# Optimization experiments

Hardware: AMD Instinct MI355X
Metric: run time of the kernel (lower is better)

The kernel has to match this reference:

```python
import jax, jax.numpy as jnp
from jax import lax
import numpy as np

TAU = 1.0          # epoch buffer = 0 -> tau_init * decay^0 = 1.0
NEG = -1.0e9
K_HOP = 2
MAX_CLUSTERS = 16
SIZE_MAX = 8
SIZE_MIN = 1
THRESH = 0.95
EPS = 1e-8


def _gumbel_hard(key, logits, m):
    # torch: logits*mask + (1-mask)*-1e9; gumbel noise; softmax; straight-through one-hot
    mf = m.astype(logits.dtype)
    ml = logits * mf + (1.0 - mf) * NEG
    u = jax.random.uniform(key, logits.shape, dtype=logits.dtype)
    g = -jnp.log(-jnp.log(u + EPS) + EPS)
    soft = jax.nn.softmax((ml + g) / TAU, axis=-1)
    idx = jnp.argmax(soft, axis=-1)
    hard = jax.nn.one_hot(idx, logits.shape[-1], dtype=logits.dtype)
    return hard + soft - lax.stop_gradient(soft), idx


def _k_hop(adj, seed_idx, m):
    # vectorized BFS via masked bmm, fixed K_HOP iterations
    N = adj.shape[1]
    seed = jax.nn.one_hot(seed_idx, N, dtype=bool)
    reach, cur = seed, seed
    for _ in range(K_HOP):
        nb = (jnp.einsum('bn,bnm->bm', cur.astype(adj.dtype), adj) > 0) & m
        new = nb & (~reach)
        reach = reach | nb
        cur = new
    return reach


def _topk_gumbel(key, logits, k, m):
    # iterative hard gumbel selection of up to k nodes per batch (k: [B] int)
    sel = jnp.zeros_like(logits)
    remaining = m
    for step in range(SIZE_MAX - SIZE_MIN):
        key, sk = jax.random.split(key)
        active = (step < k) & remaining.any(-1)
        step_mask = remaining & active[:, None]
        s, _ = _gumbel_hard(sk, logits, step_mask)
        sel = sel + s * active[:, None].astype(sel.dtype)
        remaining = remaining & ~(lax.stop_gradient(s) > 0.5)
    return sel


def _gru_seq(hist, h0, Wih, Whh, bih, bhh):
    # torch nn.GRU cell math, scan over time; hist [B,T,D], h0 [B,H]
    H = h0.shape[-1]
    def step(h, xt):
        gi = xt @ Wih.T + bih
        gh = h @ Whh.T + bhh
        r = jax.nn.sigmoid(gi[:, :H] + gh[:, :H])
        z = jax.nn.sigmoid(gi[:, H:2 * H] + gh[:, H:2 * H])
        n = jnp.tanh(gi[:, 2 * H:] + r * gh[:, 2 * H:])
        return (1.0 - z) * n + z * h, None
    h_final, _ = lax.scan(step, h0, jnp.swapaxes(hist, 0, 1))
    return h_final


def _forward(x, adj, mask, sel_w1, sel_b1, sel_w2, sel_b2,
             size_w1, size_b1, size_w2, size_b2,
             gru_wih, gru_whh, gru_bih, gru_bhh, init_w, init_b):
    B, N, D = x.shape
    H = init_w.shape[0]
    maskf = mask.astype(x.dtype)
    total = maskf.sum(-1)                                   # [B]
    x_mean = (x * maskf[:, :, None]).sum(1) / (total[:, None] + EPS)
    ctx_hidden = x_mean @ init_w.T + init_b                 # [B,H]
    global_ctx = ctx_hidden
    assignment = jnp.zeros((B, N, MAX_CLUSTERS), x.dtype)
    assigned = jnp.zeros((B, N), bool)
    history = []
    key = jax.random.key(42)
    size_range = jnp.arange(SIZE_MAX - SIZE_MIN + 1)
    for c in range(MAX_CLUSTERS):
        # gradient-safe early termination: mask contributions instead of breaking
        pct = assignment.sum((1, 2)) / (total + EPS)
        active = (pct < THRESH) & (total > 0)
        avail = mask & (~assigned)
        # selection MLP on [x, context]
        sel_in = jnp.concatenate(
            [x, jnp.broadcast_to(global_ctx[:, None, :], (B, N, H))], -1)
        h1 = jax.nn.relu(sel_in @ sel_w1.T + sel_b1)
        logits = (h1 @ sel_w2.T + sel_b2)[..., 0]           # [B,N]
        key, k1, k2, k3 = jax.random.split(key, 4)
        seed_sel, seed_idx = _gumbel_hard(k1, logits, avail)
        seed_feat = jnp.einsum('bn,bnd->bd', seed_sel, x)
        khop = _k_hop(adj, seed_idx, avail)
        candidates = khop & avail
        max_possible = jnp.minimum(candidates.sum(-1), SIZE_MAX)
        # cluster-size prediction
        size_in = jnp.concatenate(
            [seed_feat, global_ctx, max_possible.astype(x.dtype)[:, None]], -1)
        sh = jax.nn.relu(size_in @ size_w1.T + size_b1)
        size_logits = sh @ size_w2.T + size_b2              # [B,8]
        valid_ranges = jnp.clip(max_possible - SIZE_MIN + 1, 1, size_logits.shape[-1])
        range_mask = size_range[None, :] < valid_ranges[:, None]
        size_sel, _ = _gumbel_hard(k2, size_logits, range_mask)
        sizes = jnp.argmax(size_sel, -1) + SIZE_MIN         # [B]
        seed_oh = jax.nn.one_hot(seed_idx, N, dtype=bool)
        extra = _topk_gumbel(k3, logits, sizes - 1, candidates & (~seed_oh))
        cluster_sel = (seed_sel + extra) * active.astype(x.dtype)[:, None]
        assignment = assignment.at[:, :, c].set(cluster_sel)
        assigned = assigned | (lax.stop_gradient(cluster_sel) > 0.5)
        # gradient-safe cluster embedding (mean over selected nodes)
        csize = jnp.maximum(lax.stop_gradient(cluster_sel).sum(-1), 1.0)
        emb = jnp.einsum('bn,bnd->bd', cluster_sel, x) / csize[:, None]
        emb = emb * active.astype(x.dtype)[:, None]
        history.append(emb)
        # update_context_safe: rerun GRU on full history from current hidden
        hist = jnp.stack(history, 1)                        # [B,t+1,D]
        ctx_hidden = _gru_seq(hist, ctx_hidden, gru_wih, gru_whh, gru_bih, gru_bhh)
        global_ctx = ctx_hidden
    return assignment


def setup_inputs() -> dict:
    key = jax.random.key(0)
    ks = jax.random.split(key, 16)
    B, N, D, H = 32, 512, 128, 128
    x = jax.random.normal(ks[0], (B, N, D), jnp.float32)
    a = (jax.random.uniform(ks[1], (B, N, N)) < 0.02).astype(jnp.float32)
    adj = jnp.maximum(a, jnp.swapaxes(a, 1, 2))             # symmetric binary contacts
    mask = jnp.ones((B, N), bool)
    s = 0.05
    p = lambda k, sh: jax.random.normal(k, sh, jnp.float32) * s
    return dict(
        x=x, adj=adj, mask=mask,
        sel_w1=p(ks[2], (H, D + H)), sel_b1=p(ks[3], (H,)),
        sel_w2=p(ks[4], (1, H)), sel_b2=p(ks[5], (1,)),
        size_w1=p(ks[6], (H, D + H + 1)), size_b1=p(ks[7], (H,)),
        size_w2=p(ks[8], (SIZE_MAX, H)), size_b2=p(ks[9], (SIZE_MAX,)),
        gru_wih=p(ks[10], (3 * H, D)), gru_whh=p(ks[11], (3 * H, H)),
        gru_bih=p(ks[12], (3 * H,)), gru_bhh=p(ks[13], (3 * H,)),
        init_w=p(ks[14], (H, D)), init_b=p(ks[15], (H,)))


def reference(x, adj, mask, sel_w1, sel_b1, sel_w2, sel_b2,
              size_w1, size_b1, size_w2, size_b2,
              gru_wih, gru_whh, gru_bih, gru_bhh, init_w, init_b):
    return _forward(x, adj, mask, sel_w1, sel_b1, sel_w2, sel_b2,
                    size_w1, size_b1, size_w2, size_b2,
                    gru_wih, gru_whh, gru_bih, gru_bhh, init_w, init_b)
```

## Files before the change

kernel.cpp:

```cpp
#include <hip/hip_runtime.h>
#include <stdint.h>


#define NBATCH 32
#define NNODE  512
#define NDIM   128
#define NHID   128
#define NCLUS  16
#define NEGV   (-1.0e9f)
#define EPSF   (1e-8f)

struct KeyPack {
  uint32_t k1[NCLUS][2];
  uint32_t k2[NCLUS][2];
  uint32_t sk[NCLUS][7][2];
};

__host__ __device__ inline void tf2x32(uint32_t k0, uint32_t k1,
                                       uint32_t x0, uint32_t x1,
                                       uint32_t& o0, uint32_t& o1) {
  uint32_t k2 = k0 ^ k1 ^ 0x1BD11BDAu;
#define TFR(r) { x0 += x1; x1 = (x1 << (r)) | (x1 >> (32 - (r))); x1 ^= x0; }
  x0 += k0; x1 += k1;
  TFR(13) TFR(15) TFR(26) TFR(6)
  x0 += k1; x1 += k2 + 1u;
  TFR(17) TFR(29) TFR(16) TFR(24)
  x0 += k2; x1 += k0 + 2u;
  TFR(13) TFR(15) TFR(26) TFR(6)
  x0 += k0; x1 += k1 + 3u;
  TFR(17) TFR(29) TFR(16) TFR(24)
  x0 += k1; x1 += k2 + 4u;
  TFR(13) TFR(15) TFR(26) TFR(6)
  x0 += k2; x1 += k0 + 5u;
#undef TFR
  o0 = x0; o1 = x1;
}

__device__ __forceinline__ float jax_uniform(uint32_t k0, uint32_t k1, uint32_t j) {
  uint32_t a, b;
  tf2x32(k0, k1, 0u, j, a, b);
  uint32_t bits = a ^ b;
  return __uint_as_float((bits >> 9) | 0x3F800000u) - 1.0f;
}

__device__ __forceinline__ float gumb(float u) {
  return -logf(-logf(u + EPSF) + EPSF);
}

__device__ __forceinline__ float sigmf(float v) { return 1.0f / (1.0f + expf(-v)); }

__device__ __forceinline__ int block_argmax512(float v, int idx,
                                               float* rv, int* ri, int* res) {
  const int lane = threadIdx.x & 63;
  const int wid  = threadIdx.x >> 6;
#pragma unroll
  for (int off = 32; off > 0; off >>= 1) {
    float ov = __shfl_down(v, off);
    int   oi = __shfl_down(idx, off);
    if (ov > v || (ov == v && oi < idx)) { v = ov; idx = oi; }
  }
  if (lane == 0) { rv[wid] = v; ri[wid] = idx; }
  __syncthreads();
  if (threadIdx.x < 64) {
    float bv = (lane < 8) ? rv[lane] : -3.4e38f;
    int   bi = (lane < 8) ? ri[lane] : 0x7fffffff;
#pragma unroll
    for (int off = 4; off > 0; off >>= 1) {
      float ov = __shfl_down(bv, off);
      int   oi = __shfl_down(bi, off);
      if (ov > bv || (ov == bv && oi < bi)) { bv = ov; bi = oi; }
    }
    if (lane == 0) *res = bi;
  }
  __syncthreads();
  return *res;
}


__global__ void k_transpose(const float* __restrict__ gwih,
                            const float* __restrict__ gwhh,
                            const float* __restrict__ selw1, const float* __restrict__ szw1,
                            const float* __restrict__ initw,
                            float4* __restrict__ Wi3, float4* __restrict__ W3,
                            float* __restrict__ W1cT, float* __restrict__ szW1T,
                            float* __restrict__ initWT) {
  int t = blockIdx.x * blockDim.x + threadIdx.x;
  if (t < 32 * 384) {
    int i = t % 384, j4 = t / 384;
    const float* si = gwih + i * 128 + j4 * 4;
    Wi3[t] = make_float4(si[0], si[1], si[2], si[3]);
    const float* sh = gwhh + i * 128 + j4 * 4;
    W3[t]  = make_float4(sh[0], sh[1], sh[2], sh[3]);
  }
  if (t < 128 * 128) {
    int j = t >> 7, hh = t & 127;
    W1cT[t]   = selw1[hh * 256 + 128 + j];
    initWT[t] = initw[hh * 128 + j];
  }
  if (t < 257 * 128) {
    int j = t >> 7, i = t & 127;
    szW1T[t] = szw1[i * 257 + j];
  }
}

__global__ void k_adjbits(const float* __restrict__ adj, uint8_t* __restrict__ adjb8) {
  int t = blockIdx.x * blockDim.x + threadIdx.x;
  if (t >= NBATCH * NNODE * 64) return;
  const float4* p = (const float4*)adj + (size_t)t * 2;
  float4 a = p[0], b = p[1];
  uint32_t m = (a.x > 0.f ? 1u : 0u) | (a.y > 0.f ? 2u : 0u)
             | (a.z > 0.f ? 4u : 0u) | (a.w > 0.f ? 8u : 0u)
             | (b.x > 0.f ? 16u : 0u) | (b.y > 0.f ? 32u : 0u)
             | (b.z > 0.f ? 64u : 0u) | (b.w > 0.f ? 128u : 0u);
  adjb8[t] = (uint8_t)m;
}

__global__ __launch_bounds__(512)
void k_xw1(const float* __restrict__ x, const float* __restrict__ selw1,
           float* __restrict__ xw1T) {
  const int b = blockIdx.x >> 3;
  const int n0 = (blockIdx.x & 7) * 64;
  __shared__ float xs[64][NDIM + 1];
  for (int i = threadIdx.x; i < 64 * NDIM; i += 512) {
    int n = i >> 7, d = i & 127;
    xs[n][d] = x[((size_t)b * NNODE + n0 + n) * NDIM + d];
  }
  __syncthreads();
  for (int p = threadIdx.x; p < 64 * NHID; p += 512) {
    int h = p >> 6, n = p & 63;
    const float* wr = selw1 + h * 256;
    float a0 = 0.f, a1 = 0.f, a2 = 0.f, a3 = 0.f;
#pragma unroll 8
    for (int d = 0; d < NDIM; d += 4) {
      a0 = fmaf(xs[n][d + 0], wr[d + 0], a0);
      a1 = fmaf(xs[n][d + 1], wr[d + 1], a1);
      a2 = fmaf(xs[n][d + 2], wr[d + 2], a2);
      a3 = fmaf(xs[n][d + 3], wr[d + 3], a3);
    }
    xw1T[((size_t)b * NHID + h) * NNODE + n0 + n] = (a0 + a1) + (a2 + a3);
  }
}


#define MV384_PARTIALS(WP4, V4, PART)                                        \
  {                                                                          \
    const float4 cv0 = (V4)[wid * 4 + 0], cv1 = (V4)[wid * 4 + 1];           \
    const float4 cv2 = (V4)[wid * 4 + 2], cv3 = (V4)[wid * 4 + 3];           \
    _Pragma("unroll")                                                        \
    for (int m = 0; m < 6; m++) {                                            \
      const int row = lane + 64 * m;                                         \
      float4 w0 = (WP4)[row], w1 = (WP4)[384 + row];                         \
      float4 w2 = (WP4)[768 + row], w3v = (WP4)[1152 + row];                 \
      float pa = w0.x * cv0.x, pb = w0.y * cv0.y;                            \
      pa = fmaf(w0.z, cv0.z, pa);  pb = fmaf(w0.w, cv0.w, pb);               \
      pa = fmaf(w1.x, cv1.x, pa);  pb = fmaf(w1.y, cv1.y, pb);               \
      pa = fmaf(w1.z, cv1.z, pa);  pb = fmaf(w1.w, cv1.w, pb);               \
      pa = fmaf(w2.x, cv2.x, pa);  pb = fmaf(w2.y, cv2.y, pb);               \
      pa = fmaf(w2.z, cv2.z, pa);  pb = fmaf(w2.w, cv2.w, pb);               \
      pa = fmaf(w3v.x, cv3.x, pa); pb = fmaf(w3v.y, cv3.y, pb);              \
      pa = fmaf(w3v.z, cv3.z, pa); pb = fmaf(w3v.w, cv3.w, pb);              \
      (PART)[wid * 384 + row] = pa + pb;                                     \
    }                                                                        \
  }

__global__ __launch_bounds__(512)
void k_main(const float* __restrict__ x,
            const float* __restrict__ selb1, const float* __restrict__ selw2,
            const float* __restrict__ selb2,
            const float* __restrict__ szb1, const float* __restrict__ szw2,
            const float* __restrict__ szb2,
            const float* __restrict__ gbih, const float* __restrict__ gbhh,
            const float* __restrict__ initb,
            const float* __restrict__ xw1T, const uint32_t* __restrict__ adjb,
            const float4* __restrict__ Wi3, const float4* __restrict__ W3,
            const float* __restrict__ W1cT, const float* __restrict__ szW1T,
            const float* __restrict__ initWT,
            float* __restrict__ out, KeyPack kp)
{
  const int b = blockIdx.x;
  const int t = threadIdx.x;
  const int lane = t & 63, wid = t >> 6;

  __shared__ __align__(16) float ctxb[2][NHID];
  __shared__ __align__(16) float ctxterm[NHID];
  __shared__ __align__(16) float gic[NCLUS][3 * NHID];
  __shared__ __align__(16) float cat256[2 * NHID];
  __shared__ __align__(16) float embs[NDIM];
  __shared__ __align__(16) float h1s[NHID];
  __shared__ __align__(16) float xm[NHID];
  __shared__ __align__(16) float part[8 * 384];
  __shared__ __align__(16) float selw2s[NHID];
  __shared__ __align__(16) float szw2s[8 * NHID];
  __shared__ float slog[8];
  __shared__ float rv[8];
  __shared__ int   ri[8];
  __shared__ int   ibox[4];
  __shared__ uint32_t curm[16];
  __shared__ uint32_t selm[16];

  if (t < NHID) selw2s[t] = selw2[t];
  for (int i = t; i < 8 * NHID; i += 512) szw2s[i] = szw2[i];
  const float selb2_r = selb2[0];
  const float szb2_r  = szb2[wid];
  const float selb1_r = (t < NHID) ? selb1[t] : 0.f;
  const float szb1_r  = (t < NHID) ? szb1[t] : 0.f;
  const float szw1mp_r = (t < NHID) ? szW1T[256 * NHID + t] : 0.f;
  const float gbih_r  = (t < 384) ? gbih[t] : 0.f;
  float gb0 = 0.f, gb1 = 0.f, gb2 = 0.f;
  if (t < NHID) { gb0 = gbhh[t]; gb1 = gbhh[NHID + t]; gb2 = gbhh[2 * NHID + t]; }

  {
    const int j = t & 127, p = t >> 7;
    const float* xp = x + ((size_t)b * NNODE + p * 128) * NDIM + j;
    float a0 = 0.f, a1 = 0.f, a2 = 0.f, a3 = 0.f;
#pragma unroll 4
    for (int n = 0; n < 128; n += 4) {
      a0 += xp[(size_t)(n + 0) * NDIM];
      a1 += xp[(size_t)(n + 1) * NDIM];
      a2 += xp[(size_t)(n + 2) * NDIM];
      a3 += xp[(size_t)(n + 3) * NDIM];
    }
    part[p * 128 + j] = (a0 + a1) + (a2 + a3);
  }
  __syncthreads();
  if (t < NHID) xm[t] = (part[t] + part[128 + t] + part[256 + t] + part[384 + t]) * (1.0f / 512.0f);
  __syncthreads();
  if (t < NHID) {
    float a = initb[t];
    const float4* x4 = (const float4*)xm;
#pragma unroll 8
    for (int j4 = 0; j4 < 32; j4++) {
      float4 v = x4[j4];
      int j = 4 * j4;
      a = fmaf(v.x, initWT[(j + 0) * NHID + t], a);
      a = fmaf(v.y, initWT[(j + 1) * NHID + t], a);
      a = fmaf(v.z, initWT[(j + 2) * NHID + t], a);
      a = fmaf(v.w, initWT[(j + 3) * NHID + t], a);
    }
    ctxb[0][t] = a;
  }
  __syncthreads();

  int cur = 0;
  bool assigned = false;
  uint32_t selbits = 0u;

  for (int c = 0; c < NCLUS; c++) {
    {
      const int hh = t & 127, p = t >> 7;
      const float4* c4 = (const float4*)(ctxb[cur] + p * 32);
      float a0 = 0.f, a1 = 0.f, a2 = 0.f, a3 = 0.f;
#pragma unroll
      for (int j4 = 0; j4 < 8; j4++) {
        float4 cv = c4[j4];
        int j = p * 32 + j4 * 4;
        a0 = fmaf(cv.x, W1cT[(j + 0) * NHID + hh], a0);
        a1 = fmaf(cv.y, W1cT[(j + 1) * NHID + hh], a1);
        a2 = fmaf(cv.z, W1cT[(j + 2) * NHID + hh], a2);
        a3 = fmaf(cv.w, W1cT[(j + 3) * NHID + hh], a3);
      }
      part[p * 128 + hh] = (a0 + a1) + (a2 + a3);
    }
    __syncthreads();
    if (t < NHID) ctxterm[t] = selb1_r + part[t] + part[128 + t] + part[256 + t] + part[384 + t];
    __syncthreads();

    float myLogit;
    {
      float acc0 = selb2_r, acc1 = 0.f, acc2 = 0.f, acc3 = 0.f;
      const float* xp = xw1T + (size_t)b * NHID * NNODE + t;
      const float4* ct4 = (const float4*)ctxterm;
      const float4* w24 = (const float4*)selw2s;
#pragma unroll 8
      for (int h4 = 0; h4 < 32; h4++) {
        float4 cv = ct4[h4], wv = w24[h4];
        int h = h4 * 4;
        acc0 = fmaf(fmaxf(xp[(size_t)(h + 0) * NNODE] + cv.x, 0.f), wv.x, acc0);
        acc1 = fmaf(fmaxf(xp[(size_t)(h + 1) * NNODE] + cv.y, 0.f), wv.y, acc1);
        acc2 = fmaf(fmaxf(xp[(size_t)(h + 2) * NNODE] + cv.z, 0.f), wv.z, acc2);
        acc3 = fmaf(fmaxf(xp[(size_t)(h + 3) * NNODE] + cv.w, 0.f), wv.w, acc3);
      }
      myLogit = (acc0 + acc1) + (acc2 + acc3);
    }

    const bool avail = !assigned;
    float z = (avail ? myLogit : NEGV)
            + gumb(jax_uniform(kp.k1[c][0], kp.k1[c][1], (uint32_t)(b * NNODE + t)));
    const int seed = block_argmax512(z, t, rv, ri, &ibox[0]);

    bool reach = (t == seed);
    if (t < 16) curm[t] = ((seed >> 5) == t) ? (1u << (seed & 31)) : 0u;
    __syncthreads();
    const uint32_t* arow = adjb + ((size_t)b * NNODE + t) * 16;
    for (int hop = 0; hop < 2; hop++) {
      uint32_t mr = 0u;
#pragma unroll
      for (int w = 0; w < 16; w++) mr |= arow[w] & curm[w];
      const bool nb = (mr != 0u) && avail;
      const bool nw = nb && !reach;
      reach = reach || nb;
      __syncthreads();
      unsigned long long bal = __ballot(nw);
      if (lane == 0) { curm[wid * 2] = (uint32_t)bal; curm[wid * 2 + 1] = (uint32_t)(bal >> 32); }
      __syncthreads();
    }
    const bool cand = reach && avail;
    {
      unsigned long long cb = __ballot(cand);
      if (lane == 0) ri[wid] = __popcll(cb);
      __syncthreads();
      if (t == 0) { int s = 0; for (int w = 0; w < 8; w++) s += ri[w]; ibox[1] = s; }
      __syncthreads();
    }
    const int candcnt = ibox[1];
    const int mp = min(candcnt, 8);

    if (t < NHID) {
      cat256[t]        = x[((size_t)b * NNODE + seed) * NDIM + t];
      cat256[NHID + t] = ctxb[cur][t];
    }
    __syncthreads();
    {
      const int hh = t & 127, p = t >> 7;
      const float4* c4 = (const float4*)(cat256 + p * 64);
      float a0 = 0.f, a1 = 0.f, a2 = 0.f, a3 = 0.f;
#pragma unroll
      for (int j4 = 0; j4 < 16; j4++) {
        float4 cv = c4[j4];
        int j = p * 64 + j4 * 4;
        a0 = fmaf(cv.x, szW1T[(j + 0) * NHID + hh], a0);
        a1 = fmaf(cv.y, szW1T[(j + 1) * NHID + hh], a1);
        a2 = fmaf(cv.z, szW1T[(j + 2) * NHID + hh], a2);
        a3 = fmaf(cv.w, szW1T[(j + 3) * NHID + hh], a3);
      }
      part[p * 128 + hh] = (a0 + a1) + (a2 + a3);
    }
    __syncthreads();
    if (t < NHID) {
      float a = szb1_r + ((part[t] + part[128 + t]) + (part[256 + t] + part[384 + t]))
              + (float)mp * szw1mp_r;
      h1s[t] = fmaxf(a, 0.f);
    }
    __syncthreads();
    {
      float a = h1s[lane] * szw2s[wid * NHID + lane]
              + h1s[64 + lane] * szw2s[wid * NHID + 64 + lane];
#pragma unroll
      for (int off = 32; off > 0; off >>= 1) a += __shfl_down(a, off);
      if (lane == 0) {
        float g2 = gumb(jax_uniform(kp.k2[c][0], kp.k2[c][1], (uint32_t)(b * 8 + wid)));
        slog[wid] = ((wid < mp) ? (a + szb2_r) : NEGV) + g2;
      }
    }
    __syncthreads();
    if (t == 0) {
      float bv = slog[0]; int bi = 0;
      for (int q = 1; q < 8; q++) if (slog[q] > bv) { bv = slog[q]; bi = q; }
      ibox[2] = bi;
    }
    __syncthreads();
    const int kextra = ibox[2];

    bool sel = (t == seed);
    bool remaining = cand && !sel;
    int remcnt = candcnt - 1;
    int selcnt = 1;
    for (int s = 0; s < kextra; s++) {
      if (remcnt <= 0) break;
      float z3 = (remaining ? myLogit : NEGV)
               + gumb(jax_uniform(kp.sk[c][s][0], kp.sk[c][s][1], (uint32_t)(b * NNODE + t)));
      const int pick = block_argmax512(z3, t, rv, ri, &ibox[3]);
      if (t == pick) { sel = true; remaining = false; }
      remcnt--; selcnt++;
    }

    if (sel) selbits |= (1u << c);
    assigned = assigned || sel;

    {
      unsigned long long sb = __ballot(sel);
      if (lane == 0) { selm[wid * 2] = (uint32_t)sb; selm[wid * 2 + 1] = (uint32_t)(sb >> 32); }
    }
    __syncthreads();
    if (t < NDIM) {
      float a = 0.f;
      for (int w = 0; w < 16; w++) {
        uint32_t mwd = selm[w];
        while (mwd) {
          int bit = __ffs(mwd) - 1;
          mwd &= mwd - 1;
          a += x[((size_t)b * NNODE + (w * 32 + bit)) * NDIM + t];
        }
      }
      embs[t] = a / (float)selcnt;
    }
    __syncthreads();

    {
      uintptr_t wp = (uintptr_t)Wi3;
      asm volatile("" : "+s"(wp));
      const float4* wi = (const float4*)wp + (size_t)wid * 4 * 384;
      const float4* e4 = (const float4*)embs;
      MV384_PARTIALS(wi, e4, part)
    }
    __syncthreads();
    if (t < 384) {
      gic[c][t] = gbih_r
                + (((part[t] + part[384 + t]) + (part[768 + t] + part[1152 + t]))
                 + ((part[1536 + t] + part[1920 + t]) + (part[2304 + t] + part[2688 + t])));
    }
    __syncthreads();

    for (int tt = 0; tt <= c; tt++) {
      {
        uintptr_t wp = (uintptr_t)W3;
        asm volatile("" : "+s"(wp));
        const float4* w3p = (const float4*)wp + (size_t)wid * 4 * 384;
        const float4* c4 = (const float4*)ctxb[cur];
        MV384_PARTIALS(w3p, c4, part)
      }
      __syncthreads();
      if (t < NHID) {
        float ghr = ((part[t]        + part[384 + t])  + (part[768 + t]  + part[1152 + t]))
                  + ((part[1536 + t] + part[1920 + t]) + (part[2304 + t] + part[2688 + t]));
        float ghz = ((part[128 + t]  + part[512 + t])  + (part[896 + t]  + part[1280 + t]))
                  + ((part[1664 + t] + part[2048 + t]) + (part[2432 + t] + part[2816 + t]));
        float ghn = ((part[256 + t]  + part[640 + t])  + (part[1024 + t] + part[1408 + t]))
                  + ((part[1792 + t] + part[2176 + t]) + (part[2560 + t] + part[2944 + t]));
        const float* gi = gic[tt];
        float r  = sigmf(gi[t] + ghr + gb0);
        float zz = sigmf(gi[NHID + t] + ghz + gb1);
        float nn = tanhf(gi[2 * NHID + t] + r * (ghn + gb2));
        ctxb[cur ^ 1][t] = (1.f - zz) * nn + zz * ctxb[cur][t];
      }
      __syncthreads();
      cur ^= 1;
    }
  }

  float4* o4 = (float4*)(out + ((size_t)b * NNODE + t) * NCLUS);
#pragma unroll
  for (int q = 0; q < 4; q++) {
    float4 v;
    v.x = (selbits >> (4 * q + 0)) & 1u ? 1.f : 0.f;
    v.y = (selbits >> (4 * q + 1)) & 1u ? 1.f : 0.f;
    v.z = (selbits >> (4 * q + 2)) & 1u ? 1.f : 0.f;
    v.w = (selbits >> (4 * q + 3)) & 1u ? 1.f : 0.f;
    o4[q] = v;
  }
}


extern "C" void kernel_launch(void* const* d_in, const int* in_sizes, int n_in,
                              void* d_out, int out_size, void* d_ws, size_t ws_size,
                              hipStream_t stream) {
  (void)in_sizes; (void)n_in; (void)out_size; (void)ws_size;

  const float* x     = (const float*)d_in[0];
  const float* adj   = (const float*)d_in[1];
  const float* selw1 = (const float*)d_in[3];
  const float* selb1 = (const float*)d_in[4];
  const float* selw2 = (const float*)d_in[5];
  const float* selb2 = (const float*)d_in[6];
  const float* szw1  = (const float*)d_in[7];
  const float* szb1  = (const float*)d_in[8];
  const float* szw2  = (const float*)d_in[9];
  const float* szb2  = (const float*)d_in[10];
  const float* gwih  = (const float*)d_in[11];
  const float* gwhh  = (const float*)d_in[12];
  const float* gbih  = (const float*)d_in[13];
  const float* gbhh  = (const float*)d_in[14];
  const float* initw = (const float*)d_in[15];
  const float* initb = (const float*)d_in[16];
  float* out = (float*)d_out;

  float*    xw1T   = (float*)d_ws;
  uint32_t* adjb   = (uint32_t*)(xw1T + (size_t)NBATCH * NHID * NNODE);
  float*    Wi3    = (float*)(adjb + (size_t)NBATCH * NNODE * 16);
  float*    W3     = Wi3 + 384 * 128;
  float*    W1cT   = W3 + 384 * 128;
  float*    szW1T  = W1cT + 128 * 128;
  float*    initWT = szW1T + 257 * 128;

  KeyPack kp;
  uint32_t kk0 = 0u, kk1 = 42u;
  for (int c = 0; c < NCLUS; c++) {
    uint32_t nk0, nk1, t0, t1, u0, u1;
    tf2x32(kk0, kk1, 0u, 0u, nk0, nk1);
    tf2x32(kk0, kk1, 0u, 1u, kp.k1[c][0], kp.k1[c][1]);
    tf2x32(kk0, kk1, 0u, 2u, kp.k2[c][0], kp.k2[c][1]);
    tf2x32(kk0, kk1, 0u, 3u, t0, t1);
    for (int s = 0; s < 7; s++) {
      tf2x32(t0, t1, 0u, 1u, kp.sk[c][s][0], kp.sk[c][s][1]);
      tf2x32(t0, t1, 0u, 0u, u0, u1);
      t0 = u0; t1 = u1;
    }
    kk0 = nk0; kk1 = nk1;
  }

  k_transpose<<<192, 256, 0, stream>>>(gwih, gwhh, selw1, szw1, initw,
                                       (float4*)Wi3, (float4*)W3,
                                       W1cT, szW1T, initWT);
  k_adjbits<<<(NBATCH * NNODE * 64) / 256, 256, 0, stream>>>(adj, (uint8_t*)adjb);
  k_xw1<<<NBATCH * 8, 512, 0, stream>>>(x, selw1, xw1T);
  k_main<<<NBATCH, 512, 0, stream>>>(x, selb1, selw2, selb2, szb1, szw2, szb2,
                                     gbih, gbhh, initb, xw1T, adjb,
                                     (const float4*)Wi3, (const float4*)W3,
                                     W1cT, szW1T, initWT, out, kp);
}
```

Measured before the change: 740.7 us.

## Move BFS and top-k selection into one wave and cache GRU weights in LDS

The seed argmax, two-hop BFS and iterative top-k gumbel selection now run inside a single wavefront using bitmask words and shuffles. The per-step block-wide argmax reductions and their barriers are gone, and all gumbel noise is precomputed into shared memory up front. The GRU recurrence keeps half of the hidden-to-hidden weight matrix resident in LDS, double-buffers its partial sums, and passes the new hidden state between steps through register shuffles instead of a shared ping-pong buffer, so each step needs one barrier instead of two. Shared memory use grows sharply, which limits residency, and the serial selection work now runs on a single wave.

```diff
diff --git a/kernel.cpp b/kernel.cpp
--- a/kernel.cpp
+++ b/kernel.cpp
@@ -48,33 +48,6 @@
 }
 
 __device__ __forceinline__ float sigmf(float v) { return 1.0f / (1.0f + expf(-v)); }
-
-__device__ __forceinline__ int block_argmax512(float v, int idx,
-                                               float* rv, int* ri, int* res) {
-  const int lane = threadIdx.x & 63;
-  const int wid  = threadIdx.x >> 6;
-#pragma unroll
-  for (int off = 32; off > 0; off >>= 1) {
-    float ov = __shfl_down(v, off);
-    int   oi = __shfl_down(idx, off);
-    if (ov > v || (ov == v && oi < idx)) { v = ov; idx = oi; }
-  }
-  if (lane == 0) { rv[wid] = v; ri[wid] = idx; }
-  __syncthreads();
-  if (threadIdx.x < 64) {
-    float bv = (lane < 8) ? rv[lane] : -3.4e38f;
-    int   bi = (lane < 8) ? ri[lane] : 0x7fffffff;
-#pragma unroll
-    for (int off = 4; off > 0; off >>= 1) {
-      float ov = __shfl_down(bv, off);
-      int   oi = __shfl_down(bi, off);
-      if (ov > bv || (ov == bv && oi < bi)) { bv = ov; bi = oi; }
-    }
-    if (lane == 0) *res = bi;
-  }
-  __syncthreads();
-  return *res;
-}
 
 
 __global__ void k_transpose(const float* __restrict__ gwih,
@@ -181,33 +154,38 @@
   const int t = threadIdx.x;
   const int lane = t & 63, wid = t >> 6;
 
-  __shared__ __align__(16) float ctxb[2][NHID];
+  __shared__ __align__(16) float4 resW[6144];
+  __shared__ __align__(16) float gic[NCLUS][3 * NHID];
+  __shared__ __align__(16) float partf[6144];
+  __shared__ __align__(16) float gbhh_s[384];
+  __shared__ __align__(16) float ctxb[NHID];
   __shared__ __align__(16) float ctxterm[NHID];
-  __shared__ __align__(16) float gic[NCLUS][3 * NHID];
   __shared__ __align__(16) float cat256[2 * NHID];
   __shared__ __align__(16) float embs[NDIM];
   __shared__ __align__(16) float h1s[NHID];
   __shared__ __align__(16) float xm[NHID];
-  __shared__ __align__(16) float part[8 * 384];
   __shared__ __align__(16) float selw2s[NHID];
-  __shared__ __align__(16) float szw2s[8 * NHID];
   __shared__ float slog[8];
-  __shared__ float rv[8];
-  __shared__ int   ri[8];
   __shared__ int   ibox[4];
+  __shared__ uint32_t availw[16];
   __shared__ uint32_t curm[16];
   __shared__ uint32_t selm[16];
 
+#pragma unroll
+  for (int i = 0; i < 12; i++) {
+    int idx = i * 512 + t;
+    int dch = idx / 384, row = idx % 384;
+    int sj4 = 4 * (dch >> 1) + (dch & 1);
+    resW[idx] = W3[(size_t)sj4 * 384 + row];
+  }
+  if (t < 384) gbhh_s[t] = gbhh[t];
   if (t < NHID) selw2s[t] = selw2[t];
-  for (int i = t; i < 8 * NHID; i += 512) szw2s[i] = szw2[i];
   const float selb2_r = selb2[0];
   const float szb2_r  = szb2[wid];
   const float selb1_r = (t < NHID) ? selb1[t] : 0.f;
   const float szb1_r  = (t < NHID) ? szb1[t] : 0.f;
   const float szw1mp_r = (t < NHID) ? szW1T[256 * NHID + t] : 0.f;
   const float gbih_r  = (t < 384) ? gbih[t] : 0.f;
-  float gb0 = 0.f, gb1 = 0.f, gb2 = 0.f;
-  if (t < NHID) { gb0 = gbhh[t]; gb1 = gbhh[NHID + t]; gb2 = gbhh[2 * NHID + t]; }
 
   {
     const int j = t & 127, p = t >> 7;
@@ -220,10 +198,10 @@
       a2 += xp[(size_t)(n + 2) * NDIM];
       a3 += xp[(size_t)(n + 3) * NDIM];
     }
-    part[p * 128 + j] = (a0 + a1) + (a2 + a3);
+    partf[p * 128 + j] = (a0 + a1) + (a2 + a3);
   }
   __syncthreads();
-  if (t < NHID) xm[t] = (part[t] + part[128 + t] + part[256 + t] + part[384 + t]) * (1.0f / 512.0f);
+  if (t < NHID) xm[t] = (partf[t] + partf[128 + t] + partf[256 + t] + partf[384 + t]) * (1.0f / 512.0f);
   __syncthreads();
   if (t < NHID) {
     float a = initb[t];
@@ -237,18 +215,17 @@
       a = fmaf(v.z, initWT[(j + 2) * NHID + t], a);
       a = fmaf(v.w, initWT[(j + 3) * NHID + t], a);
     }
-    ctxb[0][t] = a;
+    ctxb[t] = a;
   }
   __syncthreads();
 
-  int cur = 0;
   bool assigned = false;
   uint32_t selbits = 0u;
 
   for (int c = 0; c < NCLUS; c++) {
     {
       const int hh = t & 127, p = t >> 7;
-      const float4* c4 = (const float4*)(ctxb[cur] + p * 32);
+      const float4* c4 = (const float4*)(ctxb + p * 32);
       float a0 = 0.f, a1 = 0.f, a2 = 0.f, a3 = 0.f;
 #pragma unroll
       for (int j4 = 0; j4 < 8; j4++) {
@@ -259,10 +236,10 @@
         a2 = fmaf(cv.z, W1cT[(j + 2) * NHID + hh], a2);
         a3 = fmaf(cv.w, W1cT[(j + 3) * NHID + hh], a3);
       }
-      part[p * 128 + hh] = (a0 + a1) + (a2 + a3);
-    }
-    __syncthreads();
-    if (t < NHID) ctxterm[t] = selb1_r + part[t] + part[128 + t] + part[256 + t] + part[384 + t];
+      partf[p * 128 + hh] = (a0 + a1) + (a2 + a3);
+    }
+    __syncthreads();
+    if (t < NHID) ctxterm[t] = selb1_r + partf[t] + partf[128 + t] + partf[256 + t] + partf[384 + t];
     __syncthreads();
 
     float myLogit;
@@ -282,44 +259,94 @@
       }
       myLogit = (acc0 + acc1) + (acc2 + acc3);
     }
-
-    const bool avail = !assigned;
-    float z = (avail ? myLogit : NEGV)
-            + gumb(jax_uniform(kp.k1[c][0], kp.k1[c][1], (uint32_t)(b * NNODE + t)));
-    const int seed = block_argmax512(z, t, rv, ri, &ibox[0]);
-
-    bool reach = (t == seed);
-    if (t < 16) curm[t] = ((seed >> 5) == t) ? (1u << (seed & 31)) : 0u;
-    __syncthreads();
-    const uint32_t* arow = adjb + ((size_t)b * NNODE + t) * 16;
-    for (int hop = 0; hop < 2; hop++) {
-      uint32_t mr = 0u;
-#pragma unroll
-      for (int w = 0; w < 16; w++) mr |= arow[w] & curm[w];
-      const bool nb = (mr != 0u) && avail;
-      const bool nw = nb && !reach;
-      reach = reach || nb;
-      __syncthreads();
-      unsigned long long bal = __ballot(nw);
-      if (lane == 0) { curm[wid * 2] = (uint32_t)bal; curm[wid * 2 + 1] = (uint32_t)(bal >> 32); }
-      __syncthreads();
-    }
-    const bool cand = reach && avail;
-    {
-      unsigned long long cb = __ballot(cand);
-      if (lane == 0) ri[wid] = __popcll(cb);
-      __syncthreads();
-      if (t == 0) { int s = 0; for (int w = 0; w < 8; w++) s += ri[w]; ibox[1] = s; }
-      __syncthreads();
-    }
-    const int candcnt = ibox[1];
-    const int mp = min(candcnt, 8);
-
-    if (t < NHID) {
-      cat256[t]        = x[((size_t)b * NNODE + seed) * NDIM + t];
-      cat256[NHID + t] = ctxb[cur][t];
-    }
-    __syncthreads();
+    {
+      const bool avail = !assigned;
+      float z = (avail ? myLogit : NEGV)
+              + gumb(jax_uniform(kp.k1[c][0], kp.k1[c][1], (uint32_t)(b * NNODE + t)));
+      partf[t] = z;
+      partf[4096 + t] = myLogit;
+#pragma unroll
+      for (int s = 0; s < 7; s++)
+        partf[512 + s * 512 + t] =
+            gumb(jax_uniform(kp.sk[c][s][0], kp.sk[c][s][1], (uint32_t)(b * NNODE + t)));
+      unsigned long long ab = __ballot(!assigned);
+      if (lane == 0) { availw[2 * wid] = (uint32_t)ab; availw[2 * wid + 1] = (uint32_t)(ab >> 32); }
+    }
+    __syncthreads();
+
+    if (wid == 0) {
+      float bv = -3.4e38f; int bi = 0x7fffffff;
+#pragma unroll
+      for (int k = 0; k < 8; k++) {
+        float v = partf[lane + 64 * k];
+        if (v > bv) { bv = v; bi = lane + 64 * k; }
+      }
+#pragma unroll
+      for (int off = 32; off > 0; off >>= 1) {
+        float ov = __shfl_down(bv, off); int oi = __shfl_down(bi, off);
+        if (ov > bv || (ov == bv && oi < bi)) { bv = ov; bi = oi; }
+      }
+      const int seed = __shfl(bi, 0);
+      const float cf0 = x[((size_t)b * NNODE + seed) * NDIM + lane];
+      const float cf1 = x[((size_t)b * NNODE + seed) * NDIM + 64 + lane];
+
+      uint32_t av[16], reach[16], cw[16];
+#pragma unroll
+      for (int k = 0; k < 16; k++) av[k] = availw[k];
+#pragma unroll
+      for (int k = 0; k < 16; k++) {
+        uint32_t s0 = ((seed >> 5) == k) ? (1u << (seed & 31)) : 0u;
+        reach[k] = s0; cw[k] = s0;
+      }
+#pragma unroll
+      for (int hop = 0; hop < 2; hop++) {
+        uint32_t carrier = 0u;
+#pragma unroll
+        for (int k = 0; k < 16; k++) carrier = (lane == k) ? cw[k] : carrier;
+        uint32_t myw = __shfl(carrier, lane >> 2);
+        uint32_t mybyte = (myw >> ((lane & 3) * 8)) & 0xffu;
+        uint32_t acc[16];
+#pragma unroll
+        for (int k = 0; k < 16; k++) acc[k] = 0u;
+        while (mybyte) {
+          int b2 = __ffs(mybyte) - 1; mybyte &= mybyte - 1;
+          const uint4* r4 = (const uint4*)(adjb + ((size_t)b * NNODE + 8 * lane + b2) * 16);
+          uint4 q0 = r4[0], q1 = r4[1], q2 = r4[2], q3 = r4[3];
+          acc[0] |= q0.x; acc[1] |= q0.y; acc[2]  |= q0.z; acc[3]  |= q0.w;
+          acc[4] |= q1.x; acc[5] |= q1.y; acc[6]  |= q1.z; acc[7]  |= q1.w;
+          acc[8] |= q2.x; acc[9] |= q2.y; acc[10] |= q2.z; acc[11] |= q2.w;
+          acc[12] |= q3.x; acc[13] |= q3.y; acc[14] |= q3.z; acc[15] |= q3.w;
+        }
+#pragma unroll
+        for (int off = 1; off < 64; off <<= 1) {
+#pragma unroll
+          for (int k = 0; k < 16; k++) acc[k] |= __shfl_xor(acc[k], off);
+        }
+#pragma unroll
+        for (int k = 0; k < 16; k++) {
+          uint32_t nb = acc[k] & av[k];
+          uint32_t nw = nb & ~reach[k];
+          reach[k] |= nb;
+          cw[k] = nw;
+        }
+      }
+      int cnt = 0;
+#pragma unroll
+      for (int k = 0; k < 16; k++) cnt += __popc(reach[k]);
+      if (lane == 0) {
+        ibox[0] = seed; ibox[1] = min(cnt, 8); ibox[3] = cnt;
+#pragma unroll
+        for (int k = 0; k < 16; k++) curm[k] = reach[k];
+      }
+      cat256[lane] = cf0;
+      cat256[64 + lane] = cf1;
+    } else if (wid == 1) {
+      cat256[NHID + lane] = ctxb[lane];
+      cat256[NHID + 64 + lane] = ctxb[64 + lane];
+    }
+    __syncthreads();
+    const int mp = ibox[1];
+
     {
       const int hh = t & 127, p = t >> 7;
       const float4* c4 = (const float4*)(cat256 + p * 64);
@@ -333,18 +360,18 @@
         a2 = fmaf(cv.z, szW1T[(j + 2) * NHID + hh], a2);
         a3 = fmaf(cv.w, szW1T[(j + 3) * NHID + hh], a3);
       }
-      part[p * 128 + hh] = (a0 + a1) + (a2 + a3);
+      partf[p * 128 + hh] = (a0 + a1) + (a2 + a3);
     }
     __syncthreads();
     if (t < NHID) {
-      float a = szb1_r + ((part[t] + part[128 + t]) + (part[256 + t] + part[384 + t]))
+      float a = szb1_r + ((partf[t] + partf[128 + t]) + (partf[256 + t] + partf[384 + t]))
               + (float)mp * szw1mp_r;
       h1s[t] = fmaxf(a, 0.f);
     }
     __syncthreads();
     {
-      float a = h1s[lane] * szw2s[wid * NHID + lane]
-              + h1s[64 + lane] * szw2s[wid * NHID + 64 + lane];
+      float a = h1s[lane] * szw2[wid * NHID + lane]
+              + h1s[64 + lane] * szw2[wid * NHID + 64 + lane];
 #pragma unroll
       for (int off = 32; off > 0; off >>= 1) a += __shfl_down(a, off);
       if (lane == 0) {
@@ -353,35 +380,65 @@
       }
     }
     __syncthreads();
-    if (t == 0) {
-      float bv = slog[0]; int bi = 0;
-      for (int q = 1; q < 8; q++) if (slog[q] > bv) { bv = slog[q]; bi = q; }
-      ibox[2] = bi;
-    }
-    __syncthreads();
-    const int kextra = ibox[2];
-
-    bool sel = (t == seed);
-    bool remaining = cand && !sel;
-    int remcnt = candcnt - 1;
-    int selcnt = 1;
-    for (int s = 0; s < kextra; s++) {
-      if (remcnt <= 0) break;
-      float z3 = (remaining ? myLogit : NEGV)
-               + gumb(jax_uniform(kp.sk[c][s][0], kp.sk[c][s][1], (uint32_t)(b * NNODE + t)));
-      const int pick = block_argmax512(z3, t, rv, ri, &ibox[3]);
-      if (t == pick) { sel = true; remaining = false; }
-      remcnt--; selcnt++;
-    }
-
-    if (sel) selbits |= (1u << c);
-    assigned = assigned || sel;
-
-    {
-      unsigned long long sb = __ballot(sel);
-      if (lane == 0) { selm[wid * 2] = (uint32_t)sb; selm[wid * 2 + 1] = (uint32_t)(sb >> 32); }
-    }
-    __syncthreads();
+
+    if (wid == 0) {
+      float bv0 = slog[0]; int kextra = 0;
+#pragma unroll
+      for (int q = 1; q < 8; q++) if (slog[q] > bv0) { bv0 = slog[q]; kextra = q; }
+      const int seed = ibox[0];
+      uint32_t sw[16], remw[16];
+#pragma unroll
+      for (int k = 0; k < 16; k++) {
+        uint32_t cwv = curm[k];
+        uint32_t sb = ((seed >> 5) == k) ? (1u << (seed & 31)) : 0u;
+        sw[k] = sb;
+        remw[k] = cwv & ~sb;
+      }
+      int remcnt = ibox[3] - 1;
+      int selcnt = 1;
+      for (int s = 0; s < kextra; s++) {
+        if (remcnt <= 0) break;
+        uint32_t carrier = 0u;
+#pragma unroll
+        for (int k = 0; k < 16; k++) carrier = (lane == k) ? remw[k] : carrier;
+        uint32_t myw = __shfl(carrier, lane >> 2);
+        uint32_t mybyte = (myw >> ((lane & 3) * 8)) & 0xffu;
+        float bv = -3.4e38f; int bi = 0x7fffffff;
+#pragma unroll
+        for (int b2 = 0; b2 < 8; b2++) {
+          int n = 8 * lane + b2;
+          float g  = partf[512 + s * 512 + n];
+          float lg = partf[4096 + n];
+          float v = ((mybyte >> b2) & 1u) ? (lg + g) : (NEGV + g);
+          if (v > bv) { bv = v; bi = n; }
+        }
+#pragma unroll
+        for (int off = 32; off > 0; off >>= 1) {
+          float ov = __shfl_down(bv, off); int oi = __shfl_down(bi, off);
+          if (ov > bv || (ov == bv && oi < bi)) { bv = ov; bi = oi; }
+        }
+        const int pick = __shfl(bi, 0);
+#pragma unroll
+        for (int k = 0; k < 16; k++) {
+          uint32_t bit = ((pick >> 5) == k) ? (1u << (pick & 31)) : 0u;
+          sw[k] |= bit;
+          remw[k] &= ~bit;
+        }
+        remcnt--; selcnt++;
+      }
+      if (lane == 0) {
+#pragma unroll
+        for (int k = 0; k < 16; k++) selm[k] = sw[k];
+        ibox[2] = selcnt;
+      }
+    }
+    __syncthreads();
+
+    {
+      const bool sel = ((selm[t >> 5] >> (t & 31)) & 1u) != 0u;
+      if (sel) selbits |= (1u << c);
+      assigned = assigned || sel;
+    }
     if (t < NDIM) {
       float a = 0.f;
       for (int w = 0; w < 16; w++) {
@@ -392,7 +449,7 @@
           a += x[((size_t)b * NNODE + (w * 32 + bit)) * NDIM + t];
         }
       }
-      embs[t] = a / (float)selcnt;
+      embs[t] = a / (float)ibox[2];
     }
     __syncthreads();
 
@@ -401,41 +458,74 @@
       asm volatile("" : "+s"(wp));
       const float4* wi = (const float4*)wp + (size_t)wid * 4 * 384;
       const float4* e4 = (const float4*)embs;
-      MV384_PARTIALS(wi, e4, part)
+      MV384_PARTIALS(wi, e4, partf)
     }
     __syncthreads();
     if (t < 384) {
       gic[c][t] = gbih_r
-                + (((part[t] + part[384 + t]) + (part[768 + t] + part[1152 + t]))
-                 + ((part[1536 + t] + part[1920 + t]) + (part[2304 + t] + part[2688 + t])));
-    }
-    __syncthreads();
-
-    for (int tt = 0; tt <= c; tt++) {
-      {
-        uintptr_t wp = (uintptr_t)W3;
-        asm volatile("" : "+s"(wp));
-        const float4* w3p = (const float4*)wp + (size_t)wid * 4 * 384;
-        const float4* c4 = (const float4*)ctxb[cur];
-        MV384_PARTIALS(w3p, c4, part)
-      }
-      __syncthreads();
-      if (t < NHID) {
-        float ghr = ((part[t]        + part[384 + t])  + (part[768 + t]  + part[1152 + t]))
-                  + ((part[1536 + t] + part[1920 + t]) + (part[2304 + t] + part[2688 + t]));
-        float ghz = ((part[128 + t]  + part[512 + t])  + (part[896 + t]  + part[1280 + t]))
-                  + ((part[1664 + t] + part[2048 + t]) + (part[2432 + t] + part[2816 + t]));
-        float ghn = ((part[256 + t]  + part[640 + t])  + (part[1024 + t] + part[1408 + t]))
-                  + ((part[1792 + t] + part[2176 + t]) + (part[2560 + t] + part[2944 + t]));
-        const float* gi = gic[tt];
-        float r  = sigmf(gi[t] + ghr + gb0);
-        float zz = sigmf(gi[NHID + t] + ghz + gb1);
-        float nn = tanhf(gi[2 * NHID + t] + r * (ghn + gb2));
-        ctxb[cur ^ 1][t] = (1.f - zz) * nn + zz * ctxb[cur][t];
-      }
-      __syncthreads();
-      cur ^= 1;
-    }
+                + (((partf[t] + partf[384 + t]) + (partf[768 + t] + partf[1152 + t]))
+                 + ((partf[1536 + t] + partf[1920 + t]) + (partf[2304 + t] + partf[2688 + t])));
+    }
+    __syncthreads();
+
+    {
+      const float4* cb4 = (const float4*)ctxb;
+      float4 cv0 = cb4[wid * 4 + 0], cv1 = cb4[wid * 4 + 1];
+      float4 cv2 = cb4[wid * 4 + 2], cv3 = cb4[wid * 4 + 3];
+      for (int tt = 0; tt <= c; tt++) {
+        float* pdst = partf + ((tt & 1) ? 3072 : 0);
+        {
+          uintptr_t gwp = (uintptr_t)W3;
+          asm volatile("" : "+s"(gwp));
+          const float4* ws = (const float4*)gwp;
+#pragma unroll
+          for (int m = 0; m < 6; m++) {
+            const int row = lane + 64 * m;
+            float4 w0 = resW[(2 * wid + 0) * 384 + row];
+            float4 w1 = resW[(2 * wid + 1) * 384 + row];
+            float4 w2 = ws[(size_t)(4 * wid + 2) * 384 + row];
+            float4 w3v = ws[(size_t)(4 * wid + 3) * 384 + row];
+            float pa = w0.x * cv0.x, pb = w0.y * cv0.y;
+            pa = fmaf(w0.z, cv0.z, pa);  pb = fmaf(w0.w, cv0.w, pb);
+            pa = fmaf(w1.x, cv1.x, pa);  pb = fmaf(w1.y, cv1.y, pb);
+            pa = fmaf(w1.z, cv1.z, pa);  pb = fmaf(w1.w, cv1.w, pb);
+            pa = fmaf(w2.x, cv2.x, pa);  pb = fmaf(w2.y, cv2.y, pb);
+            pa = fmaf(w2.z, cv2.z, pa);  pb = fmaf(w2.w, cv2.w, pb);
+            pa = fmaf(w3v.x, cv3.x, pa); pb = fmaf(w3v.y, cv3.y, pb);
+            pa = fmaf(w3v.z, cv3.z, pa); pb = fmaf(w3v.w, cv3.w, pb);
+            pdst[wid * 384 + row] = pa + pb;
+          }
+        }
+        __syncthreads();
+        float nv = 0.f;
+        if (lane < 16) {
+          const int u = 16 * wid + lane;
+          const float* pp = partf + ((tt & 1) ? 3072 : 0);
+          float ghr = ((pp[u]        + pp[384 + u])  + (pp[768 + u]  + pp[1152 + u]))
+                    + ((pp[1536 + u] + pp[1920 + u]) + (pp[2304 + u] + pp[2688 + u]));
+          float ghz = ((pp[128 + u]  + pp[512 + u])  + (pp[896 + u]  + pp[1280 + u]))
+                    + ((pp[1664 + u] + pp[2048 + u]) + (pp[2432 + u] + pp[2816 + u]));
+          float ghn = ((pp[256 + u]  + pp[640 + u])  + (pp[1024 + u] + pp[1408 + u]))
+                    + ((pp[1792 + u] + pp[2176 + u]) + (pp[2560 + u] + pp[2944 + u]));
+          const float* gi = gic[tt];
+          float r  = sigmf(gi[u] + ghr + gbhh_s[u]);
+          float zz = sigmf(gi[NHID + u] + ghz + gbhh_s[NHID + u]);
+          float nn = tanhf(gi[2 * NHID + u] + r * (ghn + gbhh_s[2 * NHID + u]));
+          float4 cc = (lane & 8) ? ((lane & 4) ? cv3 : cv2) : ((lane & 4) ? cv1 : cv0);
+          float old = (lane & 2) ? ((lane & 1) ? cc.w : cc.z) : ((lane & 1) ? cc.y : cc.x);
+          nv = (1.f - zz) * nn + zz * old;
+        }
+        if (tt == c) {
+          if (lane < 16) ctxb[16 * wid + lane] = nv;
+        } else {
+          cv0 = make_float4(__shfl(nv, 0),  __shfl(nv, 1),  __shfl(nv, 2),  __shfl(nv, 3));
+          cv1 = make_float4(__shfl(nv, 4),  __shfl(nv, 5),  __shfl(nv, 6),  __shfl(nv, 7));
+          cv2 = make_float4(__shfl(nv, 8),  __shfl(nv, 9),  __shfl(nv, 10), __shfl(nv, 11));
+          cv3 = make_float4(__shfl(nv, 12), __shfl(nv, 13), __shfl(nv, 14), __shfl(nv, 15));
+        }
+      }
+    }
+    __syncthreads();
   }
 
   float4* o4 = (float4*)(out + ((size_t)b * NNODE + t) * NCLUS);
```

New measurement: 816.7 us. 1.1x slower.

## Keep half of GRU recurrent weights resident in LDS and use fast activations

Applied to the files above, without the earlier changes.

Copies the first two of every four float4 rows of the recurrent GRU weight matrix (W3) into a 96KB shared-memory buffer once at kernel start. The inner recurrence loop then reads half its weights from LDS and half from global memory, which halves the repeated global/L2 weight traffic across the many GRU steps. Sigmoid and tanh now use __expf-based fast approximations, and one FMA pair is reordered in the shared macro. In exchange the kernel uses much more LDS, and the fast math and FMA reordering slightly change rounding.

```diff
diff --git a/kernel.cpp b/kernel.cpp
--- a/kernel.cpp
+++ b/kernel.cpp
@@ -47,7 +47,15 @@
   return -logf(-logf(u + EPSF) + EPSF);
 }
 
-__device__ __forceinline__ float sigmf(float v) { return 1.0f / (1.0f + expf(-v)); }
+__device__ __forceinline__ float sigmf_fast(float v) {
+  return 1.0f / (1.0f + __expf(-v));
+}
+__device__ __forceinline__ float tanh_fast(float x) {
+  float ax = fabsf(x);
+  float e = __expf(-2.0f * ax);
+  float r = (1.0f - e) / (1.0f + e);
+  return copysignf(r, x);
+}
 
 __device__ __forceinline__ int block_argmax512(float v, int idx,
                                                float* rv, int* ri, int* res) {
@@ -154,9 +162,9 @@
       float pa = w0.x * cv0.x, pb = w0.y * cv0.y;                            \
       pa = fmaf(w0.z, cv0.z, pa);  pb = fmaf(w0.w, cv0.w, pb);               \
       pa = fmaf(w1.x, cv1.x, pa);  pb = fmaf(w1.y, cv1.y, pb);               \
-      pa = fmaf(w1.z, cv1.z, pa);  pb = fmaf(w1.w, cv1.w, pb);               \
       pa = fmaf(w2.x, cv2.x, pa);  pb = fmaf(w2.y, cv2.y, pb);               \
       pa = fmaf(w2.z, cv2.z, pa);  pb = fmaf(w2.w, cv2.w, pb);               \
+      pa = fmaf(w1.z, cv1.z, pa);  pb = fmaf(w1.w, cv1.w, pb);               \
       pa = fmaf(w3v.x, cv3.x, pa); pb = fmaf(w3v.y, cv3.y, pb);              \
       pa = fmaf(w3v.z, cv3.z, pa); pb = fmaf(w3v.w, cv3.w, pb);              \
       (PART)[wid * 384 + row] = pa + pb;                                     \
@@ -181,6 +189,7 @@
   const int t = threadIdx.x;
   const int lane = t & 63, wid = t >> 6;
 
+  __shared__ __align__(16) float4 resW[6144];
   __shared__ __align__(16) float ctxb[2][NHID];
   __shared__ __align__(16) float ctxterm[NHID];
   __shared__ __align__(16) float gic[NCLUS][3 * NHID];
@@ -198,6 +207,13 @@
   __shared__ uint32_t curm[16];
   __shared__ uint32_t selm[16];
 
+#pragma unroll
+  for (int i = 0; i < 12; i++) {
+    int idx = i * 512 + t;
+    int w = idx / 768, rem = idx % 768;
+    resW[idx] = W3[(size_t)(4 * w) * 384 + rem];
+  }
+
   if (t < NHID) selw2s[t] = selw2[t];
   for (int i = t; i < 8 * NHID; i += 512) szw2s[i] = szw2[i];
   const float selb2_r = selb2[0];
@@ -413,11 +429,29 @@
 
     for (int tt = 0; tt <= c; tt++) {
       {
-        uintptr_t wp = (uintptr_t)W3;
-        asm volatile("" : "+s"(wp));
-        const float4* w3p = (const float4*)wp + (size_t)wid * 4 * 384;
+        uintptr_t gwp = (uintptr_t)W3;
+        asm volatile("" : "+s"(gwp));
+        const float4* ws = (const float4*)gwp;
         const float4* c4 = (const float4*)ctxb[cur];
-        MV384_PARTIALS(w3p, c4, part)
+        const float4 cv0 = c4[wid * 4 + 0], cv1 = c4[wid * 4 + 1];
+        const float4 cv2 = c4[wid * 4 + 2], cv3 = c4[wid * 4 + 3];
+#pragma unroll
+        for (int m = 0; m < 6; m++) {
+          const int row = lane + 64 * m;
+          float4 w2 = ws[(size_t)(4 * wid + 2) * 384 + row];
+          float4 w3v = ws[(size_t)(4 * wid + 3) * 384 + row];
+          float4 w0 = resW[wid * 768 + row];
+          float4 w1 = resW[wid * 768 + 384 + row];
+          float pa = w0.x * cv0.x, pb = w0.y * cv0.y;
+          pa = fmaf(w0.z, cv0.z, pa);  pb = fmaf(w0.w, cv0.w, pb);
+          pa = fmaf(w1.x, cv1.x, pa);  pb = fmaf(w1.y, cv1.y, pb);
+          pa = fmaf(w2.x, cv2.x, pa);  pb = fmaf(w2.y, cv2.y, pb);
+          pa = fmaf(w2.z, cv2.z, pa);  pb = fmaf(w2.w, cv2.w, pb);
+          pa = fmaf(w1.z, cv1.z, pa);  pb = fmaf(w1.w, cv1.w, pb);
+          pa = fmaf(w3v.x, cv3.x, pa); pb = fmaf(w3v.y, cv3.y, pb);
+          pa = fmaf(w3v.z, cv3.z, pa); pb = fmaf(w3v.w, cv3.w, pb);
+          part[wid * 384 + row] = pa + pb;
+        }
       }
       __syncthreads();
       if (t < NHID) {
@@ -428,9 +462,9 @@
         float ghn = ((part[256 + t]  + part[640 + t])  + (part[1024 + t] + part[1408 + t]))
                   + ((part[1792 + t] + part[2176 + t]) + (part[2560 + t] + part[2944 + t]));
         const float* gi = gic[tt];
-        float r  = sigmf(gi[t] + ghr + gb0);
-        float zz = sigmf(gi[NHID + t] + ghz + gb1);
-        float nn = tanhf(gi[2 * NHID + t] + r * (ghn + gb2));
+        float r  = sigmf_fast(gi[t] + ghr + gb0);
+        float zz = sigmf_fast(gi[NHID + t] + ghz + gb1);
+        float nn = tanh_fast(gi[2 * NHID + t] + r * (ghn + gb2));
         ctxb[cur ^ 1][t] = (1.f - zz) * nn + zz * ctxb[cur][t];
       }
       __syncthreads();
```

New measurement: 669.8 us, median of 3. -9.6%, faster.
